# Kernel optimization log

Hardware: AMD Instinct MI355X
Metric: run time of the kernel (lower is better)

## Reference

```python
import jax, jax.numpy as jnp
import numpy as np

COMMITMENT_COST = 0.25
EPS = 1e-10


def setup_inputs() -> dict:
    key = jax.random.key(0)
    k1, k2 = jax.random.split(key)
    x = jax.random.normal(k1, (64, 4096, 64), dtype=jnp.float32)          # [B, T, D]
    embedding = jax.random.normal(k2, (512, 64), dtype=jnp.float32)       # [K, D] codebook
    return {"x": x, "embedding": embedding}


def reference(x, embedding):
    B, T, D = x.shape
    K = embedding.shape[0]
    flat = x.reshape(-1, D)                                               # [N, D]
    N = flat.shape[0]

    distances = (jnp.sum(flat * flat, axis=1, keepdims=True)
                 - 2.0 * (flat @ embedding.T)
                 + jnp.sum(embedding * embedding, axis=1))

    idx = jnp.argmin(distances, axis=1)                                   # [N] nearest code
    quantized = embedding[idx].reshape(x.shape)                           # gather lookup

    # commitment loss (EMA variant: only e_latent_loss, codebook frozen w.r.t. loss)
    e_latent_loss = jnp.mean((jax.lax.stop_gradient(quantized) - x) ** 2)
    loss = COMMITMENT_COST * e_latent_loss

    # straight-through estimator
    q_st = x + jax.lax.stop_gradient(quantized - x)

    # perplexity via scatter-add histogram of code usage
    counts = jnp.zeros((K,), dtype=x.dtype).at[idx].add(jnp.ones((), x.dtype))
    avg_probs = counts / jnp.asarray(N, x.dtype)
    perplexity = jnp.exp(-jnp.sum(avg_probs * jnp.log(avg_probs + EPS)))

    return q_st, loss, perplexity
```

## Files before the change

kernel.cpp:

```cpp
#include <hip/hip_runtime.h>
#include <math.h>

#define N_ROWS   262144
#define DIM      64
#define KCODES   512
#define MT       64
#define NTHREADS 256
#define NBLOCKS  (N_ROWS / MT)
#define XS_STRIDE 68
#define ES_STRIDE 72
#define MARGIN   2e-3f

typedef float f32x4 __attribute__((ext_vector_type(4)));
typedef short s16x8 __attribute__((ext_vector_type(8)));


__device__ __forceinline__ unsigned short f2bf(float f) {
    unsigned u = __float_as_uint(f);
    unsigned r = u + 0x7fffu + ((u >> 16) & 1u);
    return (unsigned short)(r >> 16);
}
__device__ __forceinline__ float bf2f(unsigned short h) {
    return __uint_as_float(((unsigned)h) << 16);
}

__global__ __launch_bounds__(512) void vq_prep(const float* __restrict__ emb,
                                               float* __restrict__ esq,
                                               int* __restrict__ counts,
                                               float* __restrict__ lossAdj,
                                               unsigned short* __restrict__ eh,
                                               unsigned short* __restrict__ el,
                                               unsigned* __restrict__ mask) {
    int k = threadIdx.x;
    const float* e = emb + (size_t)k * DIM;
    float s = 0.f;
    #pragma unroll
    for (int d = 0; d < DIM; ++d) s += e[d] * e[d];
    esq[k] = s;
    counts[k] = 0;
    #pragma unroll
    for (int d = 0; d < DIM; ++d) {
        float v = e[d];
        unsigned short h = f2bf(v);
        eh[k * DIM + d] = h;
        el[k * DIM + d] = f2bf(v - bf2f(h));
    }
    #pragma unroll
    for (int i = 0; i < 16; ++i) mask[k * 16 + i] = 0u;
    if (k == 0) *lossAdj = 0.f;
}

__global__ __launch_bounds__(NTHREADS, 2) void vq_main(
    const float* __restrict__ x, const float* __restrict__ emb,
    const float* __restrict__ g_esq,
    const unsigned short* __restrict__ eh_g, const unsigned short* __restrict__ el_g,
    unsigned short* __restrict__ g_idx, float* __restrict__ g_lossPart,
    unsigned* __restrict__ g_mask, float* __restrict__ out)
{
    __shared__ float xs[MT * XS_STRIDE];
    __shared__ unsigned short ehs[128 * ES_STRIDE];
    __shared__ unsigned short els[128 * ES_STRIDE];
    __shared__ float esq_s[KCODES];
    __shared__ int   idx_s[MT];
    __shared__ int   flg_s[MT];
    __shared__ float wred[4];

    const int tid  = threadIdx.x;
    const int R0   = blockIdx.x * MT;
    const int w    = tid >> 6;
    const int lane = tid & 63;
    const int m    = lane & 15;
    const int q    = lane >> 4;

    #pragma unroll
    for (int i = 0; i < 4; ++i) {
        int flat = tid + NTHREADS * i;
        int r  = flat >> 4;
        int qc = flat & 15;
        f32x4 v = *(const f32x4*)&x[(size_t)(R0 + r) * DIM + 4 * qc];
        *(f32x4*)&xs[r * XS_STRIDE + 4 * qc] = v;
    }
    esq_s[tid]       = g_esq[tid];
    esq_s[tid + 256] = g_esq[tid + 256];
    __syncthreads();

    s16x8 axh[2], axl[2];
    const int lrow = w * 16 + m;
    #pragma unroll
    for (int kc = 0; kc < 2; ++kc) {
        const float* px = &xs[lrow * XS_STRIDE + kc * 32 + q * 8];
        s16x8 h, l;
        #pragma unroll
        for (int t = 0; t < 8; ++t) {
            float v = px[t];
            unsigned short hb = f2bf(v);
            h[t] = (short)hb;
            l[t] = (short)f2bf(v - bf2f(hb));
        }
        axh[kc] = h; axl[kc] = l;
    }

    f32x4 acc[32];
    #pragma unroll
    for (int a = 0; a < 32; ++a) acc[a] = (f32x4){0.f, 0.f, 0.f, 0.f};

    for (int c = 0; c < 4; ++c) {
        if (c) __syncthreads();
        #pragma unroll
        for (int i = 0; i < 4; ++i) {
            int ch = tid + NTHREADS * i;
            int rl = ch >> 3, off = (ch & 7) * 8;
            size_t gofs = (size_t)(c * 128 + rl) * DIM + off;
            *(s16x8*)&ehs[rl * ES_STRIDE + off] = *(const s16x8*)&eh_g[gofs];
            *(s16x8*)&els[rl * ES_STRIDE + off] = *(const s16x8*)&el_g[gofs];
        }
        __syncthreads();
        #pragma unroll
        for (int ct = 0; ct < 8; ++ct) {
            const int a = c * 8 + ct;
            #pragma unroll
            for (int kc = 0; kc < 2; ++kc) {
                const int bofs = (ct * 16 + m) * ES_STRIDE + kc * 32 + q * 8;
                s16x8 bh = *(const s16x8*)&ehs[bofs];
                s16x8 bl = *(const s16x8*)&els[bofs];
                acc[a] = __builtin_amdgcn_mfma_f32_16x16x32_bf16(axh[kc], bh, acc[a], 0, 0, 0);
                acc[a] = __builtin_amdgcn_mfma_f32_16x16x32_bf16(axl[kc], bh, acc[a], 0, 0, 0);
                acc[a] = __builtin_amdgcn_mfma_f32_16x16x32_bf16(axh[kc], bl, acc[a], 0, 0, 0);
            }
        }
    }

    float b1[4], b2[4]; int i1[4];
    #pragma unroll
    for (int r = 0; r < 4; ++r) { b1[r] = 3.4e38f; b2[r] = 3.4e38f; i1[r] = 0; }
    #pragma unroll
    for (int a = 0; a < 32; ++a) {
        int col = a * 16 + m;
        float e2 = esq_s[col];
        #pragma unroll
        for (int r = 0; r < 4; ++r) {
            float dist = e2 - 2.f * acc[a][r];
            if (dist < b1[r]) { b2[r] = b1[r]; b1[r] = dist; i1[r] = col; }
            else if (dist < b2[r]) b2[r] = dist;
        }
    }
    #pragma unroll
    for (int s = 1; s < 16; s <<= 1) {
        #pragma unroll
        for (int r = 0; r < 4; ++r) {
            float ob1 = __shfl_xor(b1[r], s);
            int   oi1 = __shfl_xor(i1[r], s);
            float ob2 = __shfl_xor(b2[r], s);
            bool owin = (ob1 < b1[r]) || (ob1 == b1[r] && oi1 < i1[r]);
            float lb1 = owin ? b1[r] : ob1;
            b2[r] = fminf(fminf(b2[r], ob2), lb1);
            if (owin) { b1[r] = ob1; i1[r] = oi1; }
        }
    }
    if (m == 0) {
        #pragma unroll
        for (int r = 0; r < 4; ++r) {
            int lrw = w * 16 + q * 4 + r;
            idx_s[lrw] = i1[r];
            int f = (b2[r] - b1[r] < MARGIN) ? 1 : 0;
            flg_s[lrw] = f;
            if (f) {
                int grow = R0 + lrw;
                atomicOr(&g_mask[grow >> 5], 1u << (grow & 31));
            }
        }
    }
    __syncthreads();
    if (tid < MT) g_idx[R0 + tid] = (unsigned short)idx_s[tid];

    const int r  = tid >> 2;
    const int d0 = (tid & 3) * 16;
    float lpart = 0.f;
    if (!flg_s[r]) {
        const int ki = idx_s[r];
        const float* erow = emb + (size_t)ki * DIM;
        #pragma unroll
        for (int s4 = 0; s4 < 4; ++s4) {
            int d = d0 + 4 * s4;
            f32x4 e4 = *(const f32x4*)&erow[d];
            float xv0 = xs[r * XS_STRIDE + d + 0];
            float xv1 = xs[r * XS_STRIDE + d + 1];
            float xv2 = xs[r * XS_STRIDE + d + 2];
            float xv3 = xs[r * XS_STRIDE + d + 3];
            float f0 = e4.x - xv0, f1 = e4.y - xv1, f2 = e4.z - xv2, f3 = e4.w - xv3;
            f32x4 o = {xv0 + f0, xv1 + f1, xv2 + f2, xv3 + f3};
            *(f32x4*)&out[(size_t)(R0 + r) * DIM + d] = o;
            lpart += f0*f0 + f1*f1 + f2*f2 + f3*f3;
        }
    }
    #pragma unroll
    for (int off = 32; off > 0; off >>= 1) lpart += __shfl_down(lpart, off);
    if ((tid & 63) == 0) wred[tid >> 6] = lpart;
    __syncthreads();
    if (tid == 0) g_lossPart[blockIdx.x] = wred[0] + wred[1] + wred[2] + wred[3];
}

__global__ __launch_bounds__(256) void vq_cleanup(
    const float* __restrict__ x, const float* __restrict__ emb,
    const float* __restrict__ g_esq, unsigned short* __restrict__ g_idx,
    float* __restrict__ lossAdj, const unsigned* __restrict__ g_mask,
    float* __restrict__ out)
{
    int w    = blockIdx.x * 4 + (threadIdx.x >> 6);
    int lane = threadIdx.x & 63;
    unsigned m0 = g_mask[w * 2], m1 = g_mask[w * 2 + 1];
    unsigned long long bits = ((unsigned long long)m1 << 32) | m0;
    while (bits) {
        int b = __ffsll((unsigned long long)bits) - 1;
        bits &= bits - 1;
        int row = w * 64 + b;
        const float* xr = &x[(size_t)row * DIM];
        float best = 3.4e38f; int bidx = 0;
        #pragma unroll
        for (int j = 0; j < 8; ++j) {
            int c = lane * 8 + j;
            const float* er = &emb[(size_t)c * DIM];
            float dot = 0.f;
            #pragma unroll
            for (int d = 0; d < DIM; ++d) dot = fmaf(xr[d], er[d], dot);
            float dist = g_esq[c] - 2.f * dot;
            if (dist < best) { best = dist; bidx = c; }
        }
        #pragma unroll
        for (int s = 1; s < 64; s <<= 1) {
            float ob = __shfl_xor(best, s);
            int   oi = __shfl_xor(bidx, s);
            if (ob < best || (ob == best && oi < bidx)) { best = ob; bidx = oi; }
        }
        float xv = xr[lane];
        float ev = emb[(size_t)bidx * DIM + lane];
        float f  = ev - xv;
        out[(size_t)row * DIM + lane] = xv + f;
        float lp = f * f;
        #pragma unroll
        for (int s = 1; s < 64; s <<= 1) lp += __shfl_xor(lp, s);
        if (lane == 0) {
            atomicAdd(lossAdj, lp);
            g_idx[row] = (unsigned short)bidx;
        }
    }
}

__global__ __launch_bounds__(256) void vq_hist(const unsigned short* __restrict__ g_idx,
                                               int* __restrict__ counts) {
    __shared__ int h[KCODES];
    int t = threadIdx.x;
    h[t] = 0; h[t + 256] = 0;
    __syncthreads();
    const unsigned short* p = g_idx + (size_t)blockIdx.x * 4096;
    #pragma unroll
    for (int i = 0; i < 16; ++i)
        atomicAdd(&h[p[t + 256 * i]], 1);
    __syncthreads();
    int v0 = h[t], v1 = h[t + 256];
    if (v0) atomicAdd(&counts[t], v0);
    if (v1) atomicAdd(&counts[t + 256], v1);
}

__global__ __launch_bounds__(512) void vq_final(const int* __restrict__ counts,
                                                const float* __restrict__ lossPart,
                                                const float* __restrict__ lossAdj,
                                                float* __restrict__ out) {
    __shared__ float redp[8];
    __shared__ float redl[8];
    int k = threadIdx.x;
    float p = (float)counts[k] * (1.f / 262144.f);
    float t = p * logf(p + 1e-10f);
    float l = 0.f;
    #pragma unroll
    for (int i = 0; i < 8; ++i) l += lossPart[k + 512 * i];
    #pragma unroll
    for (int off = 32; off > 0; off >>= 1) {
        t += __shfl_down(t, off);
        l += __shfl_down(l, off);
    }
    if ((k & 63) == 0) { redp[k >> 6] = t; redl[k >> 6] = l; }
    __syncthreads();
    if (k == 0) {
        float s = 0.f, ls = 0.f;
        #pragma unroll
        for (int i = 0; i < 8; ++i) { s += redp[i]; ls += redl[i]; }
        out[16777216] = (ls + *lossAdj) * (0.25f / 16777216.f);
        out[16777217] = expf(-s);
    }
}

extern "C" void kernel_launch(void* const* d_in, const int* in_sizes, int n_in,
                              void* d_out, int out_size, void* d_ws, size_t ws_size,
                              hipStream_t stream) {
    const float* x   = (const float*)d_in[0];
    const float* emb = (const float*)d_in[1];
    float* out = (float*)d_out;

    char* ws = (char*)d_ws;
    float*          esq      = (float*)(ws + 0);
    int*            counts   = (int*)(ws + 2048);
    float*          lossAdj  = (float*)(ws + 4096);
    unsigned short* eh       = (unsigned short*)(ws + 4608);
    unsigned short* el       = (unsigned short*)(ws + 70144);
    unsigned*       mask     = (unsigned*)(ws + 135680);
    unsigned short* gidx     = (unsigned short*)(ws + 168448);
    float*          lossPart = (float*)(ws + 692736);

    vq_prep<<<1, 512, 0, stream>>>(emb, esq, counts, lossAdj, eh, el, mask);
    vq_main<<<NBLOCKS, NTHREADS, 0, stream>>>(x, emb, esq, eh, el,
                                              gidx, lossPart, mask, out);
    vq_cleanup<<<1024, 256, 0, stream>>>(x, emb, esq, gidx, lossAdj, mask, out);
    vq_hist<<<64, 256, 0, stream>>>(gidx, counts);
    vq_final<<<1, 512, 0, stream>>>(counts, lossPart, lossAdj, out);
}
```

Baseline: 264.2 us.

## Fuse exact-recheck into main VQ kernel and stream argmin over codebook chunks

```diff
diff --git a/kernel.cpp b/kernel.cpp
--- a/kernel.cpp
+++ b/kernel.cpp
@@ -9,6 +9,8 @@
 #define NBLOCKS  (N_ROWS / MT)
 #define XS_STRIDE 68
 #define ES_STRIDE 72
+#define CHUNK    64
+#define NCHUNK   (KCODES / CHUNK)
 #define MARGIN   2e-3f
 
 typedef float f32x4 __attribute__((ext_vector_type(4)));
@@ -24,14 +26,13 @@
     return __uint_as_float(((unsigned)h) << 16);
 }
 
-__global__ __launch_bounds__(512) void vq_prep(const float* __restrict__ emb,
-                                               float* __restrict__ esq,
-                                               int* __restrict__ counts,
-                                               float* __restrict__ lossAdj,
-                                               unsigned short* __restrict__ eh,
-                                               unsigned short* __restrict__ el,
-                                               unsigned* __restrict__ mask) {
-    int k = threadIdx.x;
+__global__ __launch_bounds__(64) void vq_prep(const float* __restrict__ emb,
+                                              float* __restrict__ esq,
+                                              int* __restrict__ counts,
+                                              float* __restrict__ lossAdj,
+                                              unsigned short* __restrict__ eh,
+                                              unsigned short* __restrict__ el) {
+    int k = blockIdx.x * 64 + threadIdx.x;
     const float* e = emb + (size_t)k * DIM;
     float s = 0.f;
     #pragma unroll
@@ -45,24 +46,24 @@
         eh[k * DIM + d] = h;
         el[k * DIM + d] = f2bf(v - bf2f(h));
     }
-    #pragma unroll
-    for (int i = 0; i < 16; ++i) mask[k * 16 + i] = 0u;
     if (k == 0) *lossAdj = 0.f;
 }
 
-__global__ __launch_bounds__(NTHREADS, 2) void vq_main(
+__global__ __launch_bounds__(NTHREADS, 4) void vq_main(
     const float* __restrict__ x, const float* __restrict__ emb,
     const float* __restrict__ g_esq,
     const unsigned short* __restrict__ eh_g, const unsigned short* __restrict__ el_g,
     unsigned short* __restrict__ g_idx, float* __restrict__ g_lossPart,
-    unsigned* __restrict__ g_mask, float* __restrict__ out)
+    float* __restrict__ lossAdj, float* __restrict__ out)
 {
     __shared__ float xs[MT * XS_STRIDE];
-    __shared__ unsigned short ehs[128 * ES_STRIDE];
-    __shared__ unsigned short els[128 * ES_STRIDE];
+    __shared__ unsigned short ehs[CHUNK * ES_STRIDE];
+    __shared__ unsigned short els[CHUNK * ES_STRIDE];
     __shared__ float esq_s[KCODES];
     __shared__ int   idx_s[MT];
     __shared__ int   flg_s[MT];
+    __shared__ int   flist[MT];
+    __shared__ int   nflag;
     __shared__ float wred[4];
 
     const int tid  = threadIdx.x;
@@ -82,17 +83,19 @@
     }
     esq_s[tid]       = g_esq[tid];
     esq_s[tid + 256] = g_esq[tid + 256];
+    if (tid == 0) nflag = 0;
     __syncthreads();
 
     s16x8 axh[2], axl[2];
     const int lrow = w * 16 + m;
     #pragma unroll
     for (int kc = 0; kc < 2; ++kc) {
-        const float* px = &xs[lrow * XS_STRIDE + kc * 32 + q * 8];
+        f32x4 xv0 = *(const f32x4*)&xs[lrow * XS_STRIDE + kc * 32 + q * 8];
+        f32x4 xv1 = *(const f32x4*)&xs[lrow * XS_STRIDE + kc * 32 + q * 8 + 4];
         s16x8 h, l;
         #pragma unroll
         for (int t = 0; t < 8; ++t) {
-            float v = px[t];
+            float v = (t < 4) ? xv0[t] : xv1[t - 4];
             unsigned short hb = f2bf(v);
             h[t] = (short)hb;
             l[t] = (short)f2bf(v - bf2f(hb));
@@ -100,50 +103,50 @@
         axh[kc] = h; axl[kc] = l;
     }
 
-    f32x4 acc[32];
-    #pragma unroll
-    for (int a = 0; a < 32; ++a) acc[a] = (f32x4){0.f, 0.f, 0.f, 0.f};
-
-    for (int c = 0; c < 4; ++c) {
+    float b1[4], b2[4]; int i1[4];
+    #pragma unroll
+    for (int r = 0; r < 4; ++r) { b1[r] = 3.4e38f; b2[r] = 3.4e38f; i1[r] = 0; }
+
+    for (int c = 0; c < NCHUNK; ++c) {
         if (c) __syncthreads();
         #pragma unroll
-        for (int i = 0; i < 4; ++i) {
+        for (int i = 0; i < 2; ++i) {
             int ch = tid + NTHREADS * i;
             int rl = ch >> 3, off = (ch & 7) * 8;
-            size_t gofs = (size_t)(c * 128 + rl) * DIM + off;
+            size_t gofs = (size_t)(c * CHUNK + rl) * DIM + off;
             *(s16x8*)&ehs[rl * ES_STRIDE + off] = *(const s16x8*)&eh_g[gofs];
             *(s16x8*)&els[rl * ES_STRIDE + off] = *(const s16x8*)&el_g[gofs];
         }
         __syncthreads();
-        #pragma unroll
-        for (int ct = 0; ct < 8; ++ct) {
-            const int a = c * 8 + ct;
+
+        f32x4 acc[4];
+        #pragma unroll
+        for (int ct = 0; ct < 4; ++ct) acc[ct] = (f32x4){0.f, 0.f, 0.f, 0.f};
+        #pragma unroll
+        for (int ct = 0; ct < 4; ++ct) {
             #pragma unroll
             for (int kc = 0; kc < 2; ++kc) {
                 const int bofs = (ct * 16 + m) * ES_STRIDE + kc * 32 + q * 8;
                 s16x8 bh = *(const s16x8*)&ehs[bofs];
                 s16x8 bl = *(const s16x8*)&els[bofs];
-                acc[a] = __builtin_amdgcn_mfma_f32_16x16x32_bf16(axh[kc], bh, acc[a], 0, 0, 0);
-                acc[a] = __builtin_amdgcn_mfma_f32_16x16x32_bf16(axl[kc], bh, acc[a], 0, 0, 0);
-                acc[a] = __builtin_amdgcn_mfma_f32_16x16x32_bf16(axh[kc], bl, acc[a], 0, 0, 0);
+                acc[ct] = __builtin_amdgcn_mfma_f32_16x16x32_bf16(axh[kc], bh, acc[ct], 0, 0, 0);
+                acc[ct] = __builtin_amdgcn_mfma_f32_16x16x32_bf16(axl[kc], bh, acc[ct], 0, 0, 0);
+                acc[ct] = __builtin_amdgcn_mfma_f32_16x16x32_bf16(axh[kc], bl, acc[ct], 0, 0, 0);
             }
         }
-    }
-
-    float b1[4], b2[4]; int i1[4];
-    #pragma unroll
-    for (int r = 0; r < 4; ++r) { b1[r] = 3.4e38f; b2[r] = 3.4e38f; i1[r] = 0; }
-    #pragma unroll
-    for (int a = 0; a < 32; ++a) {
-        int col = a * 16 + m;
-        float e2 = esq_s[col];
-        #pragma unroll
-        for (int r = 0; r < 4; ++r) {
-            float dist = e2 - 2.f * acc[a][r];
-            if (dist < b1[r]) { b2[r] = b1[r]; b1[r] = dist; i1[r] = col; }
-            else if (dist < b2[r]) b2[r] = dist;
-        }
-    }
+        #pragma unroll
+        for (int ct = 0; ct < 4; ++ct) {
+            int col = c * CHUNK + ct * 16 + m;
+            float e2 = esq_s[col];
+            #pragma unroll
+            for (int r = 0; r < 4; ++r) {
+                float dist = e2 - 2.f * acc[ct][r];
+                if (dist < b1[r]) { b2[r] = b1[r]; b1[r] = dist; i1[r] = col; }
+                else if (dist < b2[r]) b2[r] = dist;
+            }
+        }
+    }
+
     #pragma unroll
     for (int s = 1; s < 16; s <<= 1) {
         #pragma unroll
@@ -162,16 +165,15 @@
         for (int r = 0; r < 4; ++r) {
             int lrw = w * 16 + q * 4 + r;
             idx_s[lrw] = i1[r];
-            int f = (b2[r] - b1[r] < MARGIN) ? 1 : 0;
-            flg_s[lrw] = f;
-            if (f) {
-                int grow = R0 + lrw;
-                atomicOr(&g_mask[grow >> 5], 1u << (grow & 31));
-            }
-        }
-    }
-    __syncthreads();
-    if (tid < MT) g_idx[R0 + tid] = (unsigned short)idx_s[tid];
+            flg_s[lrw] = (b2[r] - b1[r] < MARGIN) ? 1 : 0;
+        }
+    }
+    __syncthreads();
+
+    if (tid < MT) {
+        if (flg_s[tid]) { int p = atomicAdd(&nflag, 1); flist[p] = tid; }
+        else g_idx[R0 + tid] = (unsigned short)idx_s[tid];
+    }
 
     const int r  = tid >> 2;
     const int d0 = (tid & 3) * 16;
@@ -183,12 +185,9 @@
         for (int s4 = 0; s4 < 4; ++s4) {
             int d = d0 + 4 * s4;
             f32x4 e4 = *(const f32x4*)&erow[d];
-            float xv0 = xs[r * XS_STRIDE + d + 0];
-            float xv1 = xs[r * XS_STRIDE + d + 1];
-            float xv2 = xs[r * XS_STRIDE + d + 2];
-            float xv3 = xs[r * XS_STRIDE + d + 3];
-            float f0 = e4.x - xv0, f1 = e4.y - xv1, f2 = e4.z - xv2, f3 = e4.w - xv3;
-            f32x4 o = {xv0 + f0, xv1 + f1, xv2 + f2, xv3 + f3};
+            f32x4 xv = *(const f32x4*)&xs[r * XS_STRIDE + d];
+            float f0 = e4.x - xv.x, f1 = e4.y - xv.y, f2 = e4.z - xv.z, f3 = e4.w - xv.w;
+            f32x4 o = {xv.x + f0, xv.y + f1, xv.z + f2, xv.w + f3};
             *(f32x4*)&out[(size_t)(R0 + r) * DIM + d] = o;
             lpart += f0*f0 + f1*f1 + f2*f2 + f3*f3;
         }
@@ -198,33 +197,20 @@
     if ((tid & 63) == 0) wred[tid >> 6] = lpart;
     __syncthreads();
     if (tid == 0) g_lossPart[blockIdx.x] = wred[0] + wred[1] + wred[2] + wred[3];
-}
-
-__global__ __launch_bounds__(256) void vq_cleanup(
-    const float* __restrict__ x, const float* __restrict__ emb,
-    const float* __restrict__ g_esq, unsigned short* __restrict__ g_idx,
-    float* __restrict__ lossAdj, const unsigned* __restrict__ g_mask,
-    float* __restrict__ out)
-{
-    int w    = blockIdx.x * 4 + (threadIdx.x >> 6);
-    int lane = threadIdx.x & 63;
-    unsigned m0 = g_mask[w * 2], m1 = g_mask[w * 2 + 1];
-    unsigned long long bits = ((unsigned long long)m1 << 32) | m0;
-    while (bits) {
-        int b = __ffsll((unsigned long long)bits) - 1;
-        bits &= bits - 1;
-        int row = w * 64 + b;
+
+    for (int fi = w; fi < nflag; fi += 4) {
+        int row = R0 + flist[fi];
         const float* xr = &x[(size_t)row * DIM];
         float best = 3.4e38f; int bidx = 0;
         #pragma unroll
         for (int j = 0; j < 8; ++j) {
-            int c = lane * 8 + j;
-            const float* er = &emb[(size_t)c * DIM];
+            int cc = lane * 8 + j;
+            const float* er = &emb[(size_t)cc * DIM];
             float dot = 0.f;
             #pragma unroll
             for (int d = 0; d < DIM; ++d) dot = fmaf(xr[d], er[d], dot);
-            float dist = g_esq[c] - 2.f * dot;
-            if (dist < best) { best = dist; bidx = c; }
+            float dist = g_esq[cc] - 2.f * dot;
+            if (dist < best) { best = dist; bidx = cc; }
         }
         #pragma unroll
         for (int s = 1; s < 64; s <<= 1) {
@@ -303,14 +289,12 @@
     float*          lossAdj  = (float*)(ws + 4096);
     unsigned short* eh       = (unsigned short*)(ws + 4608);
     unsigned short* el       = (unsigned short*)(ws + 70144);
-    unsigned*       mask     = (unsigned*)(ws + 135680);
     unsigned short* gidx     = (unsigned short*)(ws + 168448);
     float*          lossPart = (float*)(ws + 692736);
 
-    vq_prep<<<1, 512, 0, stream>>>(emb, esq, counts, lossAdj, eh, el, mask);
+    vq_prep<<<8, 64, 0, stream>>>(emb, esq, counts, lossAdj, eh, el);
     vq_main<<<NBLOCKS, NTHREADS, 0, stream>>>(x, emb, esq, eh, el,
-                                              gidx, lossPart, mask, out);
-    vq_cleanup<<<1024, 256, 0, stream>>>(x, emb, esq, gidx, lossAdj, mask, out);
+                                              gidx, lossPart, lossAdj, out);
     vq_hist<<<64, 256, 0, stream>>>(gidx, counts);
     vq_final<<<1, 512, 0, stream>>>(counts, lossPart, lossAdj, out);
 }
```

Result: slower. 292.6 us (+10.7%).
